# Kernel optimization log

Measured on AMD Instinct MI355X. Metric: run time of the kernel, lower is better.

Reference implementation:

```python
import jax, jax.numpy as jnp
import numpy as np

N_NODES = 50000
IN_CH = 512
OUT_CH = 512
N_EDGES = 800000


def setup_inputs() -> dict:
    key = jax.random.key(0)
    ks = jax.random.split(key, 6)
    x = jax.random.normal(ks[0], (N_NODES, IN_CH), dtype=jnp.float32)
    edge_index = jax.random.randint(ks[1], (2, N_EDGES), 0, N_NODES, dtype=jnp.int64)
    edge_index_2 = jax.random.randint(ks[2], (2, N_EDGES), 0, N_NODES, dtype=jnp.int64)
    W1 = jax.random.normal(ks[3], (IN_CH, OUT_CH), dtype=jnp.float32) * (1.0 / np.sqrt(IN_CH))
    b1 = jnp.zeros((OUT_CH,), dtype=jnp.float32)
    W2 = jax.random.normal(ks[4], (IN_CH, OUT_CH), dtype=jnp.float32) * (1.0 / np.sqrt(IN_CH))
    b2 = jnp.zeros((OUT_CH,), dtype=jnp.float32)
    return {"x": x, "edge_index": edge_index, "edge_index_2": edge_index_2,
            "W1": W1, "b1": b1, "W2": W2, "b2": b2}


def _sgconv(x, edge_index, W, b, K=2):
    # PyG SGConv: K rounds of D^-1/2 (A+I) D^-1/2 propagation, then Linear.
    N = x.shape[0]
    loops = jnp.arange(N, dtype=edge_index.dtype)
    row = jnp.concatenate([edge_index[0], loops])  # source nodes
    col = jnp.concatenate([edge_index[1], loops])  # destination nodes
    deg = jax.ops.segment_sum(jnp.ones_like(col, dtype=x.dtype), col, num_segments=N)
    deg_inv_sqrt = jnp.where(deg > 0, jnp.where(deg > 0, deg, 1.0) ** -0.5, 0.0)
    norm = deg_inv_sqrt[row] * deg_inv_sqrt[col]  # [E+N]
    h = x
    for _ in range(K):
        h = jax.ops.segment_sum(h[row] * norm[:, None], col, num_segments=N)
    return h @ W + b


def reference(x, edge_index, edge_index_2, W1, b1, W2, b2):
    x1 = _sgconv(x, edge_index, W1, b1)
    x2 = _sgconv(x, edge_index_2, W2, b2)
    logits = jax.nn.softmax(x1, axis=1)
    logits_2 = jax.nn.softmax(x2, axis=1)
    predictions = jnp.argmax(logits, axis=1)
    return (logits, logits_2, predictions)
```

## Files before the change

### kernel.cpp

```cpp
#include <hip/hip_runtime.h>
#include <hip/hip_bf16.h>
#include <cstdint>
#include <cstddef>

#define N_NODES 50000
#define N_EDGES 800000
#define CH 512

typedef __attribute__((ext_vector_type(8))) short bf16x8;
typedef __attribute__((ext_vector_type(4))) float f32x4;

__device__ inline unsigned short f2b(float f) {
    __hip_bfloat16 h = __float2bfloat16(f);
    return *(unsigned short*)&h;
}
__device__ inline float blo(unsigned int u) {
    union { unsigned int i; float f; } v; v.i = u << 16; return v.f;
}
__device__ inline float bhi(unsigned int u) {
    union { unsigned int i; float f; } v; v.i = u & 0xffff0000u; return v.f;
}


__global__ __launch_bounds__(256) void count_col(const int* __restrict__ col, int* __restrict__ cnt) {
    int e = blockIdx.x * 256 + threadIdx.x;
    if (e < N_EDGES) atomicAdd(&cnt[col[e]], 1);
}

__global__ __launch_bounds__(256) void make_dinv(const int* __restrict__ cnt, float* __restrict__ dinv) {
    int i = blockIdx.x * 256 + threadIdx.x;
    if (i < N_NODES) dinv[i] = rsqrtf((float)(cnt[i] + 1));
}

__global__ __launch_bounds__(1024) void scan_offsets(const int* __restrict__ cnt, int* __restrict__ offs) {
    __shared__ int wsum[16];
    __shared__ int s_carry;
    int tid = threadIdx.x;
    int lane = tid & 63, wid = tid >> 6;
    if (tid == 0) s_carry = 0;
    __syncthreads();
    const int n = N_NODES;
    for (int c0 = 0; c0 < n; c0 += 1024) {
        int i = c0 + tid;
        int v = (i < n) ? cnt[i] : 0;
        int incl = v;
        #pragma unroll
        for (int d = 1; d < 64; d <<= 1) {
            int t = __shfl_up(incl, d, 64);
            if (lane >= d) incl += t;
        }
        if (lane == 63) wsum[wid] = incl;
        __syncthreads();
        int wbase = 0;
        for (int w = 0; w < wid; ++w) wbase += wsum[w];
        int excl = s_carry + wbase + incl - v;
        if (i < n) offs[i] = excl;
        int ctot = wbase + incl;
        __syncthreads();
        if (tid == 1023) s_carry += ctot;
        __syncthreads();
    }
    if (tid == 0) offs[n] = s_carry;
}

__global__ __launch_bounds__(256) void fill_csr(const int* __restrict__ edges,
                                                const int* __restrict__ offs,
                                                int* __restrict__ cursor,
                                                const float* __restrict__ dinv,
                                                int* __restrict__ srcs,
                                                float* __restrict__ enorm) {
    int e = blockIdx.x * 256 + threadIdx.x;
    if (e >= N_EDGES) return;
    int r = edges[e];
    int c = edges[N_EDGES + e];
    int p = offs[c] + atomicAdd(&cursor[c], 1);
    srcs[p] = r;
    enorm[p] = dinv[r] * dinv[c];
}


__global__ __launch_bounds__(256) void convert_x_bf16(const float* __restrict__ x, unsigned short* __restrict__ xb) {
    int i8 = blockIdx.x * 256 + threadIdx.x;
    const float4* x4 = (const float4*)x;
    float4 a = x4[2 * i8], b = x4[2 * i8 + 1];
    unsigned int o[4];
    o[0] = (unsigned)f2b(a.x) | ((unsigned)f2b(a.y) << 16);
    o[1] = (unsigned)f2b(a.z) | ((unsigned)f2b(a.w) << 16);
    o[2] = (unsigned)f2b(b.x) | ((unsigned)f2b(b.y) << 16);
    o[3] = (unsigned)f2b(b.z) | ((unsigned)f2b(b.w) << 16);
    ((uint4*)xb)[i8] = make_uint4(o[0], o[1], o[2], o[3]);
}

__global__ __launch_bounds__(256) void convert_w_t(const float* __restrict__ W, unsigned short* __restrict__ Wt) {
    int id = blockIdx.x * 256 + threadIdx.x;
    int k = id >> 9, n = id & 511;
    Wt[(size_t)n * 512 + k] = f2b(W[(size_t)k * 512 + n]);
}


__global__ __launch_bounds__(128) void propagate(const float* __restrict__ h, float* __restrict__ out,
                                                 const int* __restrict__ offs,
                                                 const int* __restrict__ srcs,
                                                 const float* __restrict__ enorm,
                                                 const float* __restrict__ dinv) {
    int node = blockIdx.x;
    int t = threadIdx.x;
    const float4* h4 = (const float4*)h;
    float di = dinv[node];
    float w0 = di * di;
    float4 v = h4[(size_t)node * 128 + t];
    float4 acc = make_float4(v.x * w0, v.y * w0, v.z * w0, v.w * w0);
    int e0 = offs[node], e1 = offs[node + 1];
    int e = e0;
    int eu = e0 + ((e1 - e0) & ~3);
    for (; e < eu; e += 4) {
        int s0 = srcs[e], s1 = srcs[e + 1], s2 = srcs[e + 2], s3 = srcs[e + 3];
        float wa = enorm[e], wb = enorm[e + 1], wc = enorm[e + 2], wd = enorm[e + 3];
        float4 u0 = h4[(size_t)s0 * 128 + t];
        float4 u1 = h4[(size_t)s1 * 128 + t];
        float4 u2 = h4[(size_t)s2 * 128 + t];
        float4 u3 = h4[(size_t)s3 * 128 + t];
        acc.x += u0.x * wa; acc.y += u0.y * wa; acc.z += u0.z * wa; acc.w += u0.w * wa;
        acc.x += u1.x * wb; acc.y += u1.y * wb; acc.z += u1.z * wb; acc.w += u1.w * wb;
        acc.x += u2.x * wc; acc.y += u2.y * wc; acc.z += u2.z * wc; acc.w += u2.w * wc;
        acc.x += u3.x * wd; acc.y += u3.y * wd; acc.z += u3.z * wd; acc.w += u3.w * wd;
    }
    for (; e < e1; ++e) {
        int s = srcs[e];
        float w = enorm[e];
        float4 u = h4[(size_t)s * 128 + t];
        acc.x += u.x * w; acc.y += u.y * w; acc.z += u.z * w; acc.w += u.w * w;
    }
    ((float4*)out)[(size_t)node * 128 + t] = acc;
}


__global__ __launch_bounds__(128) void propagate_bf16(const unsigned short* __restrict__ hb,
                                                      unsigned short* __restrict__ outb,
                                                      const int* __restrict__ offs,
                                                      const int* __restrict__ srcs,
                                                      const float* __restrict__ enorm,
                                                      const float* __restrict__ dinv) {
    int node = blockIdx.x * 2 + (threadIdx.x >> 6);
    int lane = threadIdx.x & 63;
    const uint4* h16 = (const uint4*)hb;
    float di = dinv[node];
    float w0 = di * di;
    float acc[8];
    uint4 sv = h16[(size_t)node * 64 + lane];
    acc[0] = blo(sv.x) * w0; acc[1] = bhi(sv.x) * w0;
    acc[2] = blo(sv.y) * w0; acc[3] = bhi(sv.y) * w0;
    acc[4] = blo(sv.z) * w0; acc[5] = bhi(sv.z) * w0;
    acc[6] = blo(sv.w) * w0; acc[7] = bhi(sv.w) * w0;
    int e0 = offs[node], e1 = offs[node + 1];
    int e = e0;
    int eu = e0 + ((e1 - e0) & ~3);
    for (; e < eu; e += 4) {
        int s0 = srcs[e], s1 = srcs[e + 1], s2 = srcs[e + 2], s3 = srcs[e + 3];
        float wa = enorm[e], wb = enorm[e + 1], wc = enorm[e + 2], wd = enorm[e + 3];
        uint4 u0 = h16[(size_t)s0 * 64 + lane];
        uint4 u1 = h16[(size_t)s1 * 64 + lane];
        uint4 u2 = h16[(size_t)s2 * 64 + lane];
        uint4 u3 = h16[(size_t)s3 * 64 + lane];
        acc[0] += blo(u0.x) * wa; acc[1] += bhi(u0.x) * wa;
        acc[2] += blo(u0.y) * wa; acc[3] += bhi(u0.y) * wa;
        acc[4] += blo(u0.z) * wa; acc[5] += bhi(u0.z) * wa;
        acc[6] += blo(u0.w) * wa; acc[7] += bhi(u0.w) * wa;
        acc[0] += blo(u1.x) * wb; acc[1] += bhi(u1.x) * wb;
        acc[2] += blo(u1.y) * wb; acc[3] += bhi(u1.y) * wb;
        acc[4] += blo(u1.z) * wb; acc[5] += bhi(u1.z) * wb;
        acc[6] += blo(u1.w) * wb; acc[7] += bhi(u1.w) * wb;
        acc[0] += blo(u2.x) * wc; acc[1] += bhi(u2.x) * wc;
        acc[2] += blo(u2.y) * wc; acc[3] += bhi(u2.y) * wc;
        acc[4] += blo(u2.z) * wc; acc[5] += bhi(u2.z) * wc;
        acc[6] += blo(u2.w) * wc; acc[7] += bhi(u2.w) * wc;
        acc[0] += blo(u3.x) * wd; acc[1] += bhi(u3.x) * wd;
        acc[2] += blo(u3.y) * wd; acc[3] += bhi(u3.y) * wd;
        acc[4] += blo(u3.z) * wd; acc[5] += bhi(u3.z) * wd;
        acc[6] += blo(u3.w) * wd; acc[7] += bhi(u3.w) * wd;
    }
    for (; e < e1; ++e) {
        int s = srcs[e];
        float w = enorm[e];
        uint4 u = h16[(size_t)s * 64 + lane];
        acc[0] += blo(u.x) * w; acc[1] += bhi(u.x) * w;
        acc[2] += blo(u.y) * w; acc[3] += bhi(u.y) * w;
        acc[4] += blo(u.z) * w; acc[5] += bhi(u.z) * w;
        acc[6] += blo(u.w) * w; acc[7] += bhi(u.w) * w;
    }
    unsigned int o0 = (unsigned)f2b(acc[0]) | ((unsigned)f2b(acc[1]) << 16);
    unsigned int o1 = (unsigned)f2b(acc[2]) | ((unsigned)f2b(acc[3]) << 16);
    unsigned int o2 = (unsigned)f2b(acc[4]) | ((unsigned)f2b(acc[5]) << 16);
    unsigned int o3 = (unsigned)f2b(acc[6]) | ((unsigned)f2b(acc[7]) << 16);
    ((uint4*)outb)[(size_t)node * 64 + lane] = make_uint4(o0, o1, o2, o3);
}


#define BM 64
#define BN 64
#define BK 16

__global__ __launch_bounds__(256) void gemm_bias(const float* __restrict__ A, const float* __restrict__ W,
                                                 const float* __restrict__ bias, float* __restrict__ C) {
    __shared__ float Ast[BK][BM + 4];
    __shared__ float Ws[BK][BN + 4];
    int tid = threadIdx.x;
    int bm = blockIdx.x * BM;
    int bn = blockIdx.y * BN;
    int tx = tid & 15, ty = tid >> 4;
    float acc[4][4] = {};

    int ar = tid >> 2;
    int ak = (tid & 3) * 4;
    int wr = tid >> 4;
    int wc = (tid & 15) * 4;
    int arow = bm + ar;
    bool aval = arow < N_NODES;

    for (int k0 = 0; k0 < CH; k0 += BK) {
        float4 av = make_float4(0.f, 0.f, 0.f, 0.f);
        if (aval) av = *(const float4*)&A[(size_t)arow * CH + k0 + ak];
        float4 wv = *(const float4*)&W[(size_t)(k0 + wr) * CH + bn + wc];
        Ast[ak + 0][ar] = av.x;
        Ast[ak + 1][ar] = av.y;
        Ast[ak + 2][ar] = av.z;
        Ast[ak + 3][ar] = av.w;
        *(float4*)&Ws[wr][wc] = wv;
        __syncthreads();
        #pragma unroll
        for (int k = 0; k < BK; ++k) {
            float4 a = *(const float4*)&Ast[k][ty * 4];
            float4 w = *(const float4*)&Ws[k][tx * 4];
            float as[4] = {a.x, a.y, a.z, a.w};
            float wsv[4] = {w.x, w.y, w.z, w.w};
            #pragma unroll
            for (int i = 0; i < 4; ++i)
                #pragma unroll
                for (int j = 0; j < 4; ++j)
                    acc[i][j] += as[i] * wsv[j];
        }
        __syncthreads();
    }

    float4 bv = *(const float4*)&bias[bn + tx * 4];
    #pragma unroll
    for (int i = 0; i < 4; ++i) {
        int row = bm + ty * 4 + i;
        if (row < N_NODES) {
            float4 o = make_float4(acc[i][0] + bv.x, acc[i][1] + bv.y,
                                   acc[i][2] + bv.z, acc[i][3] + bv.w);
            *(float4*)&C[(size_t)row * CH + bn + tx * 4] = o;
        }
    }
}


#define BM2 128
#define BN2 64
#define BK2 32
#define LDP 40

__global__ __launch_bounds__(256) void gemm_bf16(const unsigned short* __restrict__ Ab,
                                                 const unsigned short* __restrict__ Wt,
                                                 const float* __restrict__ bias,
                                                 float* __restrict__ C) {
    __shared__ short Alds[BM2 * LDP];
    __shared__ short Blds[BN2 * LDP];
    int tid = threadIdx.x;
    int lane = tid & 63;
    int wid = tid >> 6;
    int wm = wid & 1;
    int wn = wid >> 1;
    int bm = blockIdx.x * BM2;
    int bn = blockIdx.y * BN2;

    f32x4 acc[4][2] = {};

    int arow0 = tid >> 2, aq = tid & 3;
    int brow = tid >> 2, bq = tid & 3;

    for (int k0 = 0; k0 < CH; k0 += BK2) {
        #pragma unroll
        for (int h = 0; h < 2; ++h) {
            int row = arow0 + h * 64;
            int gr = bm + row;
            uint4 v = make_uint4(0u, 0u, 0u, 0u);
            if (gr < N_NODES) v = *(const uint4*)&Ab[(size_t)gr * CH + k0 + aq * 8];
            *(uint4*)&Alds[row * LDP + aq * 8] = v;
        }
        {
            uint4 v = *(const uint4*)&Wt[(size_t)(bn + brow) * CH + k0 + bq * 8];
            *(uint4*)&Blds[brow * LDP + bq * 8] = v;
        }
        __syncthreads();

        bf16x8 af[4], bf[2];
        #pragma unroll
        for (int mt = 0; mt < 4; ++mt)
            af[mt] = *(const bf16x8*)&Alds[(wm * 64 + mt * 16 + (lane & 15)) * LDP + (lane >> 4) * 8];
        #pragma unroll
        for (int nt = 0; nt < 2; ++nt)
            bf[nt] = *(const bf16x8*)&Blds[(wn * 32 + nt * 16 + (lane & 15)) * LDP + (lane >> 4) * 8];
        #pragma unroll
        for (int mt = 0; mt < 4; ++mt)
            #pragma unroll
            for (int nt = 0; nt < 2; ++nt)
                acc[mt][nt] = __builtin_amdgcn_mfma_f32_16x16x32_bf16(af[mt], bf[nt], acc[mt][nt], 0, 0, 0);
        __syncthreads();
    }

    #pragma unroll
    for (int mt = 0; mt < 4; ++mt) {
        #pragma unroll
        for (int nt = 0; nt < 2; ++nt) {
            int col = bn + wn * 32 + nt * 16 + (lane & 15);
            float bv = bias[col];
            #pragma unroll
            for (int r = 0; r < 4; ++r) {
                int row = bm + wm * 64 + mt * 16 + (lane >> 4) * 4 + r;
                if (row < N_NODES) C[(size_t)row * CH + col] = acc[mt][nt][r] + bv;
            }
        }
    }
}


__global__ __launch_bounds__(256) void softmax_rows(const float* __restrict__ X, float* __restrict__ P,
                                                    float* __restrict__ preds) {
    int row = blockIdx.x * 4 + (threadIdx.x >> 6);
    int lane = threadIdx.x & 63;
    if (row >= N_NODES) return;
    const float4* x4 = (const float4*)(X + (size_t)row * CH);
    float4 v0 = x4[lane];
    float4 v1 = x4[lane + 64];
    float vals[8] = {v0.x, v0.y, v0.z, v0.w, v1.x, v1.y, v1.z, v1.w};
    float m = vals[0];
    int mi = lane * 4;
    #pragma unroll
    for (int j = 1; j < 8; ++j) {
        int c = (j < 4) ? (lane * 4 + j) : (256 + lane * 4 + (j - 4));
        if (vals[j] > m) { m = vals[j]; mi = c; }
    }
    #pragma unroll
    for (int d = 32; d > 0; d >>= 1) {
        float om = __shfl_xor(m, d, 64);
        int oi = __shfl_xor(mi, d, 64);
        if (om > m || (om == m && oi < mi)) { m = om; mi = oi; }
    }
    float s = 0.f;
    float ex[8];
    #pragma unroll
    for (int j = 0; j < 8; ++j) { ex[j] = __expf(vals[j] - m); s += ex[j]; }
    #pragma unroll
    for (int d = 32; d > 0; d >>= 1) s += __shfl_xor(s, d, 64);
    float inv = 1.0f / s;
    float4 o0 = make_float4(ex[0] * inv, ex[1] * inv, ex[2] * inv, ex[3] * inv);
    float4 o1 = make_float4(ex[4] * inv, ex[5] * inv, ex[6] * inv, ex[7] * inv);
    float4* p4 = (float4*)(P + (size_t)row * CH);
    p4[lane] = o0;
    p4[lane + 64] = o1;
    if (preds != nullptr && lane == 0) preds[row] = (float)mi;
}


extern "C" void kernel_launch(void* const* d_in, const int* in_sizes, int n_in,
                              void* d_out, int out_size, void* d_ws, size_t ws_size,
                              hipStream_t stream) {
    const float* x  = (const float*)d_in[0];
    const int*   e1 = (const int*)d_in[1];
    const int*   e2 = (const int*)d_in[2];
    const float* W1 = (const float*)d_in[3];
    const float* b1 = (const float*)d_in[4];
    const float* W2 = (const float*)d_in[5];
    const float* b2 = (const float*)d_in[6];

    float* out     = (float*)d_out;
    float* logits1 = out;
    float* logits2 = out + (size_t)N_NODES * CH;
    float* preds   = out + 2 * (size_t)N_NODES * CH;

    const size_t NEED = 109600016;
    if (ws_size < NEED) return;

    char* ws = (char*)d_ws;
    float* A      = (float*)(ws);
    int*   cnt    = (int*)(ws + 102400000);
    int*   offs   = (int*)(ws + 102600000);
    int*   cursor = (int*)(ws + 102800016);
    float* dinv   = (float*)(ws + 103000016);
    int*   srcs   = (int*)(ws + 103200016);
    float* enorm  = (float*)(ws + 106400016);

    unsigned short* xb  = (unsigned short*)logits1;
    unsigned short* Wtb = (unsigned short*)((char*)logits1 + 51200000);
    unsigned short* h1b = (unsigned short*)A;
    unsigned short* h2b = (unsigned short*)((char*)A + 51200000);

    {
        hipMemsetAsync(cnt, 0, N_NODES * sizeof(int), stream);
        hipMemsetAsync(cursor, 0, N_NODES * sizeof(int), stream);
        count_col<<<(N_EDGES + 255) / 256, 256, 0, stream>>>(e2 + N_EDGES, cnt);
        make_dinv<<<(N_NODES + 255) / 256, 256, 0, stream>>>(cnt, dinv);
        scan_offsets<<<1, 1024, 0, stream>>>(cnt, offs);
        fill_csr<<<(N_EDGES + 255) / 256, 256, 0, stream>>>(e2, offs, cursor, dinv, srcs, enorm);

        convert_x_bf16<<<(N_NODES * CH / 8 + 255) / 256, 256, 0, stream>>>(x, xb);
        convert_w_t<<<(512 * 512) / 256, 256, 0, stream>>>(W2, Wtb);

        propagate_bf16<<<N_NODES / 2, 128, 0, stream>>>(xb, h1b, offs, srcs, enorm, dinv);
        propagate_bf16<<<N_NODES / 2, 128, 0, stream>>>(h1b, h2b, offs, srcs, enorm, dinv);

        dim3 g((N_NODES + BM2 - 1) / BM2, CH / BN2);
        gemm_bf16<<<g, 256, 0, stream>>>(h2b, Wtb, b2, logits2);
        softmax_rows<<<N_NODES / 4, 256, 0, stream>>>(logits2, logits2, nullptr);
    }

    {
        hipMemsetAsync(cnt, 0, N_NODES * sizeof(int), stream);
        hipMemsetAsync(cursor, 0, N_NODES * sizeof(int), stream);
        count_col<<<(N_EDGES + 255) / 256, 256, 0, stream>>>(e1 + N_EDGES, cnt);
        make_dinv<<<(N_NODES + 255) / 256, 256, 0, stream>>>(cnt, dinv);
        scan_offsets<<<1, 1024, 0, stream>>>(cnt, offs);
        fill_csr<<<(N_EDGES + 255) / 256, 256, 0, stream>>>(e1, offs, cursor, dinv, srcs, enorm);

        propagate<<<N_NODES, 128, 0, stream>>>(x, logits1, offs, srcs, enorm, dinv);
        propagate<<<N_NODES, 128, 0, stream>>>(logits1, A, offs, srcs, enorm, dinv);

        dim3 g((N_NODES + BM - 1) / BM, CH / BN);
        gemm_bias<<<g, 256, 0, stream>>>(A, W1, b1, logits1);
        softmax_rows<<<N_NODES / 4, 256, 0, stream>>>(logits1, logits1, preds);
    }
}
```

Before: 1.810 ms.

## Replace fp32 SIMT GEMM with split-bf16x3 MFMA GEMM plus argmax fixup

The fp32 SIMT GEMM for the first SGConv is replaced by an MFMA GEMM that splits A and W into high and low bf16 parts and accumulates three products, approximating fp32 accuracy. Softmax now also tracks the second-largest logit and records rows whose top-two gap is small. A fixup kernel recomputes those rows' logits in full fp32 to correct the argmax predictions. This trades extra conversions and a small fixup pass for much faster matrix-core throughput, at some risk to logit precision.

```diff
diff --git a/kernel.cpp b/kernel.cpp
--- a/kernel.cpp
+++ b/kernel.cpp
@@ -19,6 +19,9 @@
 }
 __device__ inline float bhi(unsigned int u) {
     union { unsigned int i; float f; } v; v.i = u & 0xffff0000u; return v.f;
+}
+__device__ inline unsigned int pack2(unsigned short a, unsigned short b) {
+    return (unsigned)a | ((unsigned)b << 16);
 }
 
 
@@ -84,10 +87,10 @@
     const float4* x4 = (const float4*)x;
     float4 a = x4[2 * i8], b = x4[2 * i8 + 1];
     unsigned int o[4];
-    o[0] = (unsigned)f2b(a.x) | ((unsigned)f2b(a.y) << 16);
-    o[1] = (unsigned)f2b(a.z) | ((unsigned)f2b(a.w) << 16);
-    o[2] = (unsigned)f2b(b.x) | ((unsigned)f2b(b.y) << 16);
-    o[3] = (unsigned)f2b(b.z) | ((unsigned)f2b(b.w) << 16);
+    o[0] = pack2(f2b(a.x), f2b(a.y));
+    o[1] = pack2(f2b(a.z), f2b(a.w));
+    o[2] = pack2(f2b(b.x), f2b(b.y));
+    o[3] = pack2(f2b(b.z), f2b(b.w));
     ((uint4*)xb)[i8] = make_uint4(o[0], o[1], o[2], o[3]);
 }
 
@@ -95,6 +98,19 @@
     int id = blockIdx.x * 256 + threadIdx.x;
     int k = id >> 9, n = id & 511;
     Wt[(size_t)n * 512 + k] = f2b(W[(size_t)k * 512 + n]);
+}
+
+__global__ __launch_bounds__(256) void convert_w_t_split(const float* __restrict__ W,
+                                                         unsigned short* __restrict__ Wth,
+                                                         unsigned short* __restrict__ Wtl) {
+    int id = blockIdx.x * 256 + threadIdx.x;
+    int k = id >> 9, n = id & 511;
+    float f = W[(size_t)k * 512 + n];
+    unsigned short hb = f2b(f);
+    union { unsigned int u; float ff; } t; t.u = (unsigned)hb << 16;
+    float lo = f - t.ff;
+    Wth[(size_t)n * 512 + k] = hb;
+    Wtl[(size_t)n * 512 + k] = f2b(lo);
 }
 
 
@@ -188,70 +204,11 @@
         acc[4] += blo(u.z) * w; acc[5] += bhi(u.z) * w;
         acc[6] += blo(u.w) * w; acc[7] += bhi(u.w) * w;
     }
-    unsigned int o0 = (unsigned)f2b(acc[0]) | ((unsigned)f2b(acc[1]) << 16);
-    unsigned int o1 = (unsigned)f2b(acc[2]) | ((unsigned)f2b(acc[3]) << 16);
-    unsigned int o2 = (unsigned)f2b(acc[4]) | ((unsigned)f2b(acc[5]) << 16);
-    unsigned int o3 = (unsigned)f2b(acc[6]) | ((unsigned)f2b(acc[7]) << 16);
+    unsigned int o0 = pack2(f2b(acc[0]), f2b(acc[1]));
+    unsigned int o1 = pack2(f2b(acc[2]), f2b(acc[3]));
+    unsigned int o2 = pack2(f2b(acc[4]), f2b(acc[5]));
+    unsigned int o3 = pack2(f2b(acc[6]), f2b(acc[7]));
     ((uint4*)outb)[(size_t)node * 64 + lane] = make_uint4(o0, o1, o2, o3);
-}
-
-
-#define BM 64
-#define BN 64
-#define BK 16
-
-__global__ __launch_bounds__(256) void gemm_bias(const float* __restrict__ A, const float* __restrict__ W,
-                                                 const float* __restrict__ bias, float* __restrict__ C) {
-    __shared__ float Ast[BK][BM + 4];
-    __shared__ float Ws[BK][BN + 4];
-    int tid = threadIdx.x;
-    int bm = blockIdx.x * BM;
-    int bn = blockIdx.y * BN;
-    int tx = tid & 15, ty = tid >> 4;
-    float acc[4][4] = {};
-
-    int ar = tid >> 2;
-    int ak = (tid & 3) * 4;
-    int wr = tid >> 4;
-    int wc = (tid & 15) * 4;
-    int arow = bm + ar;
-    bool aval = arow < N_NODES;
-
-    for (int k0 = 0; k0 < CH; k0 += BK) {
-        float4 av = make_float4(0.f, 0.f, 0.f, 0.f);
-        if (aval) av = *(const float4*)&A[(size_t)arow * CH + k0 + ak];
-        float4 wv = *(const float4*)&W[(size_t)(k0 + wr) * CH + bn + wc];
-        Ast[ak + 0][ar] = av.x;
-        Ast[ak + 1][ar] = av.y;
-        Ast[ak + 2][ar] = av.z;
-        Ast[ak + 3][ar] = av.w;
-        *(float4*)&Ws[wr][wc] = wv;
-        __syncthreads();
-        #pragma unroll
-        for (int k = 0; k < BK; ++k) {
-            float4 a = *(const float4*)&Ast[k][ty * 4];
-            float4 w = *(const float4*)&Ws[k][tx * 4];
-            float as[4] = {a.x, a.y, a.z, a.w};
-            float wsv[4] = {w.x, w.y, w.z, w.w};
-            #pragma unroll
-            for (int i = 0; i < 4; ++i)
-                #pragma unroll
-                for (int j = 0; j < 4; ++j)
-                    acc[i][j] += as[i] * wsv[j];
-        }
-        __syncthreads();
-    }
-
-    float4 bv = *(const float4*)&bias[bn + tx * 4];
-    #pragma unroll
-    for (int i = 0; i < 4; ++i) {
-        int row = bm + ty * 4 + i;
-        if (row < N_NODES) {
-            float4 o = make_float4(acc[i][0] + bv.x, acc[i][1] + bv.y,
-                                   acc[i][2] + bv.z, acc[i][3] + bv.w);
-            *(float4*)&C[(size_t)row * CH + bn + tx * 4] = o;
-        }
-    }
 }
 
 
@@ -325,8 +282,112 @@
 }
 
 
+#define BM3 128
+#define BN3 64
+#define BK3 32
+#define LDP3 40
+
+__global__ __launch_bounds__(256) void gemm_bf16x3(const float* __restrict__ A,
+                                                   const unsigned short* __restrict__ Wth,
+                                                   const unsigned short* __restrict__ Wtl,
+                                                   const float* __restrict__ bias,
+                                                   float* __restrict__ C) {
+    __shared__ short Ah[BM3 * LDP3];
+    __shared__ short Al[BM3 * LDP3];
+    __shared__ short Bh[BN3 * LDP3];
+    __shared__ short Bl[BN3 * LDP3];
+    int tid = threadIdx.x;
+    int lane = tid & 63;
+    int wid = tid >> 6;
+    int wm = wid & 1;
+    int wn = wid >> 1;
+    int bm = blockIdx.x * BM3;
+    int bn = blockIdx.y * BN3;
+
+    f32x4 acc[4][2] = {};
+
+    int arow = tid >> 1, aseg = tid & 1;
+    int ga = bm + arow;
+    bool aval = ga < N_NODES;
+    const float4* A4 = (const float4*)A;
+    int brow = tid >> 2, bq = tid & 3;
+
+    for (int k0 = 0; k0 < CH; k0 += BK3) {
+        {
+            size_t base = (size_t)ga * 128 + (k0 >> 2) + aseg * 4;
+            unsigned short h[16], l[16];
+            #pragma unroll
+            for (int v = 0; v < 4; ++v) {
+                float4 f = aval ? A4[base + v] : make_float4(0.f, 0.f, 0.f, 0.f);
+                float fs[4] = {f.x, f.y, f.z, f.w};
+                #pragma unroll
+                for (int j = 0; j < 4; ++j) {
+                    unsigned short hb = f2b(fs[j]);
+                    union { unsigned int u; float ff; } t; t.u = (unsigned)hb << 16;
+                    float lo = fs[j] - t.ff;
+                    h[v * 4 + j] = hb;
+                    l[v * 4 + j] = f2b(lo);
+                }
+            }
+            uint4 H0 = make_uint4(pack2(h[0], h[1]), pack2(h[2], h[3]), pack2(h[4], h[5]), pack2(h[6], h[7]));
+            uint4 H1 = make_uint4(pack2(h[8], h[9]), pack2(h[10], h[11]), pack2(h[12], h[13]), pack2(h[14], h[15]));
+            uint4 L0 = make_uint4(pack2(l[0], l[1]), pack2(l[2], l[3]), pack2(l[4], l[5]), pack2(l[6], l[7]));
+            uint4 L1 = make_uint4(pack2(l[8], l[9]), pack2(l[10], l[11]), pack2(l[12], l[13]), pack2(l[14], l[15]));
+            *(uint4*)&Ah[arow * LDP3 + aseg * 16] = H0;
+            *(uint4*)&Ah[arow * LDP3 + aseg * 16 + 8] = H1;
+            *(uint4*)&Al[arow * LDP3 + aseg * 16] = L0;
+            *(uint4*)&Al[arow * LDP3 + aseg * 16 + 8] = L1;
+        }
+        *(uint4*)&Bh[brow * LDP3 + bq * 8] = *(const uint4*)&Wth[(size_t)(bn + brow) * CH + k0 + bq * 8];
+        *(uint4*)&Bl[brow * LDP3 + bq * 8] = *(const uint4*)&Wtl[(size_t)(bn + brow) * CH + k0 + bq * 8];
+        __syncthreads();
+
+        bf16x8 afh[4], afl[4], bfh[2], bfl[2];
+        #pragma unroll
+        for (int mt = 0; mt < 4; ++mt) {
+            int off = (wm * 64 + mt * 16 + (lane & 15)) * LDP3 + (lane >> 4) * 8;
+            afh[mt] = *(const bf16x8*)&Ah[off];
+            afl[mt] = *(const bf16x8*)&Al[off];
+        }
+        #pragma unroll
+        for (int nt = 0; nt < 2; ++nt) {
+            int off = (wn * 32 + nt * 16 + (lane & 15)) * LDP3 + (lane >> 4) * 8;
+            bfh[nt] = *(const bf16x8*)&Bh[off];
+            bfl[nt] = *(const bf16x8*)&Bl[off];
+        }
+        #pragma unroll
+        for (int mt = 0; mt < 4; ++mt)
+            #pragma unroll
+            for (int nt = 0; nt < 2; ++nt) {
+                acc[mt][nt] = __builtin_amdgcn_mfma_f32_16x16x32_bf16(afh[mt], bfh[nt], acc[mt][nt], 0, 0, 0);
+                acc[mt][nt] = __builtin_amdgcn_mfma_f32_16x16x32_bf16(afl[mt], bfh[nt], acc[mt][nt], 0, 0, 0);
+                acc[mt][nt] = __builtin_amdgcn_mfma_f32_16x16x32_bf16(afh[mt], bfl[nt], acc[mt][nt], 0, 0, 0);
+            }
+        __syncthreads();
+    }
+
+    #pragma unroll
+    for (int mt = 0; mt < 4; ++mt) {
+        #pragma unroll
+        for (int nt = 0; nt < 2; ++nt) {
+            int col = bn + wn * 32 + nt * 16 + (lane & 15);
+            float bv = bias[col];
+            #pragma unroll
+            for (int r = 0; r < 4; ++r) {
+                int row = bm + wm * 64 + mt * 16 + (lane >> 4) * 4 + r;
+                if (row < N_NODES) C[(size_t)row * CH + col] = acc[mt][nt][r] + bv;
+            }
+        }
+    }
+}
+
+
+#define GAP_THR 1.0e-2f
+
 __global__ __launch_bounds__(256) void softmax_rows(const float* __restrict__ X, float* __restrict__ P,
-                                                    float* __restrict__ preds) {
+                                                    float* __restrict__ preds,
+                                                    int* __restrict__ susp_cnt,
+                                                    int* __restrict__ susp_rows) {
     int row = blockIdx.x * 4 + (threadIdx.x >> 6);
     int lane = threadIdx.x & 63;
     if (row >= N_NODES) return;
@@ -335,17 +396,25 @@
     float4 v1 = x4[lane + 64];
     float vals[8] = {v0.x, v0.y, v0.z, v0.w, v1.x, v1.y, v1.z, v1.w};
     float m = vals[0];
+    float m2 = -INFINITY;
     int mi = lane * 4;
     #pragma unroll
     for (int j = 1; j < 8; ++j) {
         int c = (j < 4) ? (lane * 4 + j) : (256 + lane * 4 + (j - 4));
-        if (vals[j] > m) { m = vals[j]; mi = c; }
+        if (vals[j] > m) { m2 = m; m = vals[j]; mi = c; }
+        else if (vals[j] > m2) { m2 = vals[j]; }
     }
     #pragma unroll
     for (int d = 32; d > 0; d >>= 1) {
         float om = __shfl_xor(m, d, 64);
         int oi = __shfl_xor(mi, d, 64);
-        if (om > m || (om == m && oi < mi)) { m = om; mi = oi; }
+        float om2 = __shfl_xor(m2, d, 64);
+        if (om > m || (om == m && oi < mi)) {
+            m2 = fmaxf(m, om2);
+            m = om; mi = oi;
+        } else {
+            m2 = fmaxf(m2, om);
+        }
     }
     float s = 0.f;
     float ex[8];
@@ -359,7 +428,75 @@
     float4* p4 = (float4*)(P + (size_t)row * CH);
     p4[lane] = o0;
     p4[lane + 64] = o1;
-    if (preds != nullptr && lane == 0) preds[row] = (float)mi;
+    if (preds != nullptr && lane == 0) {
+        preds[row] = (float)mi;
+        if (m - m2 < GAP_THR) {
+            int p = atomicAdd(susp_cnt, 1);
+            susp_rows[p] = row;
+        }
+    }
+}
+
+
+__global__ __launch_bounds__(256) void fix_preds(const float* __restrict__ A, const float* __restrict__ W,
+                                                 const float* __restrict__ bias,
+                                                 const int* __restrict__ susp_cnt,
+                                                 const int* __restrict__ susp_rows,
+                                                 float* __restrict__ preds) {
+    __shared__ float rowbuf[8][512];
+    __shared__ float rbest[8][4];
+    __shared__ int ridx[8][4];
+    int cnt = *susp_cnt;
+    if (cnt > N_NODES) cnt = N_NODES;
+    int tid = threadIdx.x, lane = tid & 63, wid = tid >> 6;
+    for (int base = blockIdx.x * 8; base < cnt; base += gridDim.x * 8) {
+        int nr = min(8, cnt - base);
+        __syncthreads();
+        for (int r = 0; r < nr; ++r) {
+            int row = susp_rows[base + r];
+            if (tid < 128) ((float4*)rowbuf[r])[tid] = ((const float4*)&A[(size_t)row * 512])[tid];
+        }
+        __syncthreads();
+        float best[8]; int bidx[8];
+        #pragma unroll
+        for (int r = 0; r < 8; ++r) { best[r] = -INFINITY; bidx[r] = 0; }
+        for (int cc = 0; cc < 2; ++cc) {
+            int c = cc * 256 + tid;
+            float bv = bias[c];
+            float s[8];
+            #pragma unroll
+            for (int r = 0; r < 8; ++r) s[r] = bv;
+            for (int k = 0; k < 512; ++k) {
+                float w = W[(size_t)k * 512 + c];
+                #pragma unroll
+                for (int r = 0; r < 8; ++r) s[r] += rowbuf[r][k] * w;
+            }
+            #pragma unroll
+            for (int r = 0; r < 8; ++r)
+                if (s[r] > best[r]) { best[r] = s[r]; bidx[r] = c; }
+        }
+        #pragma unroll
+        for (int r = 0; r < 8; ++r) {
+            float b = best[r]; int i = bidx[r];
+            #pragma unroll
+            for (int d = 32; d > 0; d >>= 1) {
+                float ob = __shfl_xor(b, d, 64);
+                int oi = __shfl_xor(i, d, 64);
+                if (ob > b || (ob == b && oi < i)) { b = ob; i = oi; }
+            }
+            if (lane == 0) { rbest[r][wid] = b; ridx[r][wid] = i; }
+        }
+        __syncthreads();
+        if (tid < nr) {
+            int r = tid;
+            float b = rbest[r][0]; int i = ridx[r][0];
+            #pragma unroll
+            for (int w = 1; w < 4; ++w) {
+                if (rbest[r][w] > b || (rbest[r][w] == b && ridx[r][w] < i)) { b = rbest[r][w]; i = ridx[r][w]; }
+            }
+            preds[susp_rows[base + r]] = (float)i;
+        }
+    }
 }
 
 
@@ -396,6 +533,11 @@
     unsigned short* h1b = (unsigned short*)A;
     unsigned short* h2b = (unsigned short*)((char*)A + 51200000);
 
+    unsigned short* Wt1h = (unsigned short*)srcs;
+    unsigned short* Wt1l = (unsigned short*)enorm;
+    int* susp_cnt  = (int*)cursor;
+    int* susp_rows = (int*)cursor + 1;
+
     {
         hipMemsetAsync(cnt, 0, N_NODES * sizeof(int), stream);
         hipMemsetAsync(cursor, 0, N_NODES * sizeof(int), stream);
@@ -412,7 +554,7 @@
 
         dim3 g((N_NODES + BM2 - 1) / BM2, CH / BN2);
         gemm_bf16<<<g, 256, 0, stream>>>(h2b, Wtb, b2, logits2);
-        softmax_rows<<<N_NODES / 4, 256, 0, stream>>>(logits2, logits2, nullptr);
+        softmax_rows<<<N_NODES / 4, 256, 0, stream>>>(logits2, logits2, nullptr, nullptr, nullptr);
     }
 
     {
@@ -426,8 +568,12 @@
         propagate<<<N_NODES, 128, 0, stream>>>(x, logits1, offs, srcs, enorm, dinv);
         propagate<<<N_NODES, 128, 0, stream>>>(logits1, A, offs, srcs, enorm, dinv);
 
-        dim3 g((N_NODES + BM - 1) / BM, CH / BN);
-        gemm_bias<<<g, 256, 0, stream>>>(A, W1, b1, logits1);
-        softmax_rows<<<N_NODES / 4, 256, 0, stream>>>(logits1, logits1, preds);
-    }
-}
+        convert_w_t_split<<<(512 * 512) / 256, 256, 0, stream>>>(W1, Wt1h, Wt1l);
+        hipMemsetAsync(susp_cnt, 0, sizeof(int), stream);
+
+        dim3 g((N_NODES + BM3 - 1) / BM3, CH / BN3);
+        gemm_bf16x3<<<g, 256, 0, stream>>>(A, Wt1h, Wt1l, b1, logits1);
+        softmax_rows<<<N_NODES / 4, 256, 0, stream>>>(logits1, logits1, preds, susp_cnt, susp_rows);
+        fix_preds<<<128, 256, 0, stream>>>(A, W1, b1, susp_cnt, susp_rows, preds);
+    }
+}
```

Result: slower. 3.236 ms (+78.8%).
